# Kernel optimization log

Measured on AMD Instinct MI355X. Metric: run time of the kernel, lower is better.

## Reference

```python
import jax, jax.numpy as jnp
import numpy as np

N_HEAD, N_KV, HD, CA_DIM, VE_CH = 16, 4, 64, 32, 12
B, T, C = 4, 1024, 1024
FFN_H = 4 * C
CA_STEPS = 4

def rms_norm(x):
    return x * jax.lax.rsqrt(jnp.mean(x * x, axis=-1, keepdims=True) + 1e-6)

def rope(x, cos, sin):
    d = x.shape[-1] // 2
    x1, x2 = x[..., :d], x[..., d:]
    return jnp.concatenate([x1 * cos + x2 * sin, -x1 * sin + x2 * cos], axis=-1)

def dwconv1d(x_bct, w, pad):  # w: (Cch,1,K) depthwise
    return jax.lax.conv_general_dilated(x_bct, w, (1,), [(pad, pad)],
        feature_group_count=x_bct.shape[1], dimension_numbers=('NCH', 'OIH', 'NCH'))

def dwconv2d(x_bchw, w):  # w: (Cch,1,3,3) depthwise
    return jax.lax.conv_general_dilated(x_bchw, w, (1, 1), [(1, 1), (1, 1)],
        feature_group_count=x_bchw.shape[1], dimension_numbers=('NCHW', 'OIHW', 'NCHW'))

def ca_channel(x, ca_pi, ca_cw, ca_po):
    h = x @ ca_pi.T  # (B,T,CA_DIM)
    h = h + 0.1 * jnp.transpose(dwconv1d(jnp.transpose(h, (0, 2, 1)), ca_cw, 1), (0, 2, 1))
    return jax.nn.gelu(h, approximate=False) @ ca_po.T

def setup_inputs() -> dict:
    key = jax.random.key(0)
    ks = jax.random.split(key, 20)
    s = 0.02
    pos = jnp.arange(T, dtype=jnp.float32)
    inv_freq = 1.0 / (10000.0 ** (jnp.arange(HD // 2, dtype=jnp.float32) / (HD // 2)))
    ang = pos[:, None] * inv_freq[None, :]  # (T, HD/2)
    return {
        'x': jax.random.normal(ks[0], (B, T, C), jnp.float32),
        've': jax.random.normal(ks[1], (B, T, N_KV * HD), jnp.float32),
        'cos': jnp.cos(ang)[None, :, None, :],
        'sin': jnp.sin(ang)[None, :, None, :],
        'prev_attn': jax.random.uniform(ks[2], (B, N_HEAD, T, T), jnp.float32),
        'w_q': s * jax.random.normal(ks[3], (N_HEAD * HD, C), jnp.float32),
        'w_k': s * jax.random.normal(ks[4], (N_KV * HD, C), jnp.float32),
        'w_v': s * jax.random.normal(ks[5], (N_KV * HD, C), jnp.float32),
        'w_o': s * jax.random.normal(ks[6], (C, C), jnp.float32),
        'w_ve_gate': s * jax.random.normal(ks[7], (N_KV, VE_CH), jnp.float32),
        'refine_w': s * jax.random.normal(ks[8], (N_HEAD, 1, 3, 3), jnp.float32),
        'refine_alpha': jnp.float32(0.05),
        'ca_pi': s * jax.random.normal(ks[9], (CA_DIM, C), jnp.float32),
        'ca_cw': s * jax.random.normal(ks[10], (CA_DIM, 1, 3), jnp.float32),
        'ca_po': s * jax.random.normal(ks[11], (C, CA_DIM), jnp.float32),
        'ffn_in': s * jax.random.normal(ks[12], (FFN_H, C), jnp.float32),
        'ffn_cw': s * jax.random.normal(ks[13], (FFN_H, 1, 3), jnp.float32),
        'ffn_out': s * jax.random.normal(ks[14], (C, FFN_H), jnp.float32),
        'ffn_gate': s * jax.random.normal(ks[15], (C, C), jnp.float32),
        'vit_w1': s * jax.random.normal(ks[16], (32, C), jnp.float32),
        'vit_w2': s * jax.random.normal(ks[17], (1, 32), jnp.float32),
    }

def reference(x, ve, cos, sin, prev_attn, w_q, w_k, w_v, w_o, w_ve_gate,
              refine_w, refine_alpha, ca_pi, ca_cw, ca_po,
              ffn_in, ffn_cw, ffn_out, ffn_gate, vit_w1, vit_w2):
    Bx, Tx, Cx = x.shape
    xn = rms_norm(x)
    q = (xn @ w_q.T).reshape(Bx, Tx, N_HEAD, HD)
    k = (xn @ w_k.T).reshape(Bx, Tx, N_KV, HD)
    v = (xn @ w_v.T).reshape(Bx, Tx, N_KV, HD)
    gate = 3.0 * jax.nn.sigmoid(xn[..., :VE_CH] @ w_ve_gate.T)  # (B,T,N_KV)
    v = v + gate[..., None] * ve.reshape(Bx, Tx, N_KV, HD)
    q = rms_norm(rope(q, cos, sin)) * 1.2
    k = rms_norm(rope(k, cos, sin)) * 1.2
    r = N_HEAD // N_KV
    k = jnp.repeat(k, r, axis=2)
    v = jnp.repeat(v, r, axis=2)
    q, k, v = (jnp.transpose(t, (0, 2, 1, 3)) for t in (q, k, v))  # (B,H,T,HD)
    att = jnp.einsum('bhqd,bhkd->bhqk', q, k) * (1.0 / np.sqrt(HD))
    att = att + refine_alpha * dwconv2d(prev_attn[:, :, :Tx, :Tx], refine_w)
    cmask = jnp.tril(jnp.ones((Tx, Tx), bool))
    att = jnp.where(cmask, att, -jnp.inf)
    aw = jax.nn.softmax(att, axis=-1)
    y = jnp.einsum('bhqk,bhkd->bhqd', aw, v)
    attn_out = jnp.transpose(y, (0, 2, 1, 3)).reshape(Bx, Tx, Cx) @ w_o.T
    # ca_mode='both': gate the attention output
    ca1 = ca_channel(x, ca_pi, ca_cw, ca_po)
    x1 = x + attn_out * (1.0 + 0.1 * jnp.tanh(ca1))
    # CAFFN
    xm = rms_norm(x1)
    h = jnp.square(jax.nn.relu(xm @ ffn_in.T))  # (B,T,FFN_H)
    ht = jnp.transpose(h, (0, 2, 1))
    for _ in range(CA_STEPS):
        ht = ht + 0.1 * dwconv1d(ht, ffn_cw, 1)
    h = jnp.transpose(ht, (0, 2, 1))
    mlp = (h @ ffn_out.T) * jax.nn.sigmoid(xm @ ffn_gate.T)
    ca2 = ca_channel(x1, ca_pi, ca_cw, ca_po)
    mlp = mlp * (1.0 + 0.1 * jnp.tanh(ca2))
    # vitality gating: MLP -> sigmoid, then avg_pool1d(k=5, pad=2, zero-counted)
    vit = jax.nn.sigmoid(jax.nn.gelu(x1 @ vit_w1.T, approximate=False) @ vit_w2.T)[..., 0]  # (B,T)
    vp = jnp.pad(vit, ((0, 0), (2, 2)))
    vs = sum(vp[:, i:i + Tx] for i in range(5)) / 5.0
    vit = 0.7 * vit + 0.3 * vs
    vit = jnp.where(vit > 0.3, vit, vit * 0.1)
    return x1 + mlp * vit[..., None]
```

## Files before the change

kernel.cpp:

```cpp
#include <hip/hip_runtime.h>

#define BB 4
#define TT 1024
#define CC 1024
#define NH 16
#define NKV 4
#define HD 64
#define FFNH 4096
#define CAD 32
#define TQ 64
#define TK 64

typedef short bf16x8 __attribute__((ext_vector_type(8)));
typedef float f32x4  __attribute__((ext_vector_type(4)));

#define AS1 __attribute__((address_space(1)))
#define AS3 __attribute__((address_space(3)))

__device__ __forceinline__ float sigf(float x){ return 1.f/(1.f+__expf(-x)); }
__device__ __forceinline__ float geluf(float x){ return 0.5f*x*(1.f+erff(x*0.70710678118654752f)); }

__device__ __forceinline__ unsigned short f2bf(float f){
  unsigned int u = __float_as_uint(f);
  u += 0x7fffu + ((u >> 16) & 1u);
  return (unsigned short)(u >> 16);
}
__device__ __forceinline__ float bf2f(unsigned short h){
  return __uint_as_float(((unsigned int)h) << 16);
}

__global__ __launch_bounds__(256) void rmsnorm_pair_k(const float* __restrict__ x,
    unsigned short* __restrict__ oh, unsigned short* __restrict__ ol){
  int row = blockIdx.x;
  const float* xr = x + (size_t)row * CC;
  float v[4]; float ss = 0.f;
  #pragma unroll
  for (int i = 0; i < 4; i++){ v[i] = xr[threadIdx.x + 256*i]; ss += v[i]*v[i]; }
  #pragma unroll
  for (int off = 1; off < 64; off <<= 1) ss += __shfl_xor(ss, off);
  __shared__ float red[4];
  if ((threadIdx.x & 63) == 0) red[threadIdx.x >> 6] = ss;
  __syncthreads();
  float tot = red[0]+red[1]+red[2]+red[3];
  float rs = rsqrtf(tot * (1.f/CC) + 1e-6f);
  size_t base = (size_t)row * CC;
  #pragma unroll
  for (int i = 0; i < 4; i++){
    float r = v[i]*rs;
    unsigned short h = f2bf(r);
    oh[base + threadIdx.x + 256*i] = h;
    ol[base + threadIdx.x + 256*i] = f2bf(r - bf2f(h));
  }
}

__global__ __launch_bounds__(256) void split_k(const float* __restrict__ in,
    unsigned short* __restrict__ hi, unsigned short* __restrict__ lo, int n4){
  int i = blockIdx.x*256 + threadIdx.x;
  if (i >= n4) return;
  float4 v = ((const float4*)in)[i];
  unsigned short h0 = f2bf(v.x), h1 = f2bf(v.y), h2v = f2bf(v.z), h3 = f2bf(v.w);
  ushort4 hv = { h0, h1, h2v, h3 };
  ushort4 lv = { f2bf(v.x - bf2f(h0)), f2bf(v.y - bf2f(h1)),
                 f2bf(v.z - bf2f(h2v)), f2bf(v.w - bf2f(h3)) };
  ((ushort4*)hi)[i] = hv;
  ((ushort4*)lo)[i] = lv;
}

template<int EPI>
__global__ __launch_bounds__(256) void gemm3_k(
    const unsigned short* __restrict__ Ah, const unsigned short* __restrict__ Al,
    const unsigned short* __restrict__ Wh, const unsigned short* __restrict__ Wl,
    float* __restrict__ C, int M, int N, int K, int KC)
{
  __shared__ unsigned short AhS[128*32];
  __shared__ unsigned short AlS[128*32];
  __shared__ unsigned short WhS[128*32];
  __shared__ unsigned short WlS[128*32];
  int tid  = threadIdx.x;
  int lane = tid & 63, wave = tid >> 6;
  int wr = wave >> 1, wc = wave & 1;
  int m0 = blockIdx.y << 7, n0 = blockIdx.x << 7;
  int z  = blockIdx.z;
  int kbase = z * KC;
  float* Cz = C + (size_t)z * M * N;
  int lr = lane & 15, lc = lane >> 4;

  int offA[4], offB[4];
  #pragma unroll
  for (int m = 0; m < 4; m++){
    int row = wr*64 + m*16 + lr;
    offA[m] = row*64 + ((lc ^ ((row >> 1) & 3)) << 4);
  }
  #pragma unroll
  for (int n = 0; n < 4; n++){
    int row = wc*64 + n*16 + lr;
    offB[n] = row*64 + ((lc ^ ((row >> 1) & 3)) << 4);
  }

  f32x4 acc[4][4] = {};

  for (int k0 = kbase; k0 < kbase + KC; k0 += 32){
    __syncthreads();
    {
      const unsigned short* srcs[4] = { Ah, Al, Wh, Wl };
      unsigned short* dsts[4] = { AhS, AlS, WhS, WlS };
      int rb[4] = { m0, m0, n0, n0 };
      #pragma unroll
      for (int tle = 0; tle < 4; tle++){
        #pragma unroll
        for (int i = 0; i < 2; i++){
          int s = i*256 + tid;
          int row = s >> 2;
          int c = (s & 3) ^ ((row >> 1) & 3);
          const unsigned short* gp = srcs[tle] + (size_t)(rb[tle] + row)*K + (k0 + c*8);
          unsigned short* lp = dsts[tle] + i*2048 + wave*512;
          __builtin_amdgcn_global_load_lds((const AS1 void*)gp, (AS3 void*)lp, 16, 0, 0);
        }
      }
    }
    __syncthreads();

    bf16x8 ah[4], al[4], bh[4], bl[4];
    #pragma unroll
    for (int m = 0; m < 4; m++){
      ah[m] = *(const bf16x8*)((const char*)AhS + offA[m]);
      al[m] = *(const bf16x8*)((const char*)AlS + offA[m]);
    }
    #pragma unroll
    for (int n = 0; n < 4; n++){
      bh[n] = *(const bf16x8*)((const char*)WhS + offB[n]);
      bl[n] = *(const bf16x8*)((const char*)WlS + offB[n]);
    }
    #pragma unroll
    for (int m = 0; m < 4; m++){
      #pragma unroll
      for (int n = 0; n < 4; n++){
        acc[m][n] = __builtin_amdgcn_mfma_f32_16x16x32_bf16(al[m], bh[n], acc[m][n], 0, 0, 0);
        acc[m][n] = __builtin_amdgcn_mfma_f32_16x16x32_bf16(ah[m], bl[n], acc[m][n], 0, 0, 0);
        acc[m][n] = __builtin_amdgcn_mfma_f32_16x16x32_bf16(ah[m], bh[n], acc[m][n], 0, 0, 0);
      }
    }
  }

  #pragma unroll
  for (int m = 0; m < 4; m++){
    int r0 = m0 + wr*64 + m*16 + lc*4;
    #pragma unroll
    for (int n = 0; n < 4; n++){
      int col = n0 + wc*64 + n*16 + lr;
      #pragma unroll
      for (int r = 0; r < 4; r++){
        float z2 = acc[m][n][r];
        if (EPI == 1){ z2 = fmaxf(z2, 0.f); z2 = z2*z2; }
        Cz[(size_t)(r0 + r)*N + col] = z2;
      }
    }
  }
}

__global__ __launch_bounds__(256) void redsum_k(const float* __restrict__ p,
    float* __restrict__ o, size_t n, int parts){
  size_t i = ((size_t)blockIdx.x*256 + threadIdx.x)*4;
  float4 s = *(const float4*)(p + i);
  for (int z = 1; z < parts; z++){
    float4 q = *(const float4*)(p + (size_t)z*n + i);
    s.x += q.x; s.y += q.y; s.z += q.z; s.w += q.w;
  }
  *(float4*)(o + i) = s;
}

__global__ __launch_bounds__(64) void rope_rms_k(float* __restrict__ q,
    const float* __restrict__ cs, const float* __restrict__ sn, int nh){
  int idx = blockIdx.x;
  int t = (idx / nh) & (TT-1);
  float* qp = q + (size_t)idx * HD;
  int d = threadIdx.x;
  int dl = d & 31;
  float c = cs[t*32 + dl], s = sn[t*32 + dl];
  float v0 = qp[d];
  float vp = qp[(d < 32) ? d + 32 : d - 32];
  float r = (d < 32) ? (v0*c + vp*s) : (v0*c - vp*s);
  float ss = r*r;
  #pragma unroll
  for (int off = 1; off < 64; off <<= 1) ss += __shfl_xor(ss, off);
  float rs = rsqrtf(ss*(1.f/HD) + 1e-6f) * 1.2f;
  qp[d] = r*rs;
}

__global__ __launch_bounds__(256) void gatev_k(float* __restrict__ v,
    const unsigned short* __restrict__ xnh, const unsigned short* __restrict__ xnl,
    const float* __restrict__ ve, const float* __restrict__ wg){
  int bt = blockIdx.x;
  int tid = threadIdx.x;
  int kv = tid >> 6;
  float s = 0.f;
  #pragma unroll
  for (int j = 0; j < 12; j++){
    float xv = bf2f(xnh[(size_t)bt*CC + j]) + bf2f(xnl[(size_t)bt*CC + j]);
    s += xv*wg[kv*12+j];
  }
  float gate = 3.f * sigf(s);
  size_t i = (size_t)bt*(NKV*HD) + tid;
  v[i] += gate * ve[i];
}

__global__ __launch_bounds__(256) void fattn_k(
    const float* __restrict__ q, const float* __restrict__ k, const float* __restrict__ v,
    const float* __restrict__ pa, const float* __restrict__ rw,
    const float* __restrict__ alphap,
    unsigned short* __restrict__ yh, unsigned short* __restrict__ yl)
{
  int qt = blockIdx.x;
  int h  = blockIdx.y;
  int b  = blockIdx.z;
  int kv = h >> 2;
  int t0 = qt * TQ;
  int tid = threadIdx.x;
  int lane = tid & 63, w = tid >> 6;
  int dl = lane & 15, gq = lane >> 4;

  __shared__ __align__(16) unsigned short Kh[4096], Kl[4096];
  __shared__ __align__(16) unsigned short Vh[64][68];
  __shared__ __align__(16) unsigned short SBs[66*68];
  __shared__ __align__(16) unsigned short Ph[4][1024];

  bf16x8 qfh[2], qfl[2];
  {
    const float* qrow = q + (((size_t)(b*TT + t0 + 16*w + dl))*NH + h)*HD;
    #pragma unroll
    for (int ks = 0; ks < 2; ks++){
      float4 a = *(const float4*)(qrow + (gq+4*ks)*8);
      float4 bq = *(const float4*)(qrow + (gq+4*ks)*8 + 4);
      float vv[8] = {a.x,a.y,a.z,a.w,bq.x,bq.y,bq.z,bq.w};
      #pragma unroll
      for (int i = 0; i < 8; i++){
        unsigned short hv = f2bf(vv[i]);
        qfh[ks][i] = (short)hv;
        qfl[ks][i] = (short)f2bf(vv[i] - bf2f(hv));
      }
    }
  }

  float alpha = *alphap;
  float w9[9];
  #pragma unroll
  for (int j = 0; j < 9; j++) w9[j] = rw[h*9+j]*alpha;

  float m_i = -1e30f, l_i = 0.f;
  f32x4 acc_o[4] = {};
  int ql = 16*w + dl;

  for (int kt = 0; kt <= qt; kt++){
    int k0 = kt*TK;
    __syncthreads();
    #pragma unroll
    for (int it = 0; it < 4; it++){
      int s = it*256 + tid;
      int r = s >> 4, d4 = (s & 15) << 2;
      const float* kp = k + (((size_t)(b*TT + k0 + r))*NKV + kv)*HD + d4;
      float4 val = *(const float4*)kp;
      ushort4 hv = { f2bf(val.x), f2bf(val.y), f2bf(val.z), f2bf(val.w) };
      ushort4 lv = { f2bf(val.x - bf2f(hv.x)), f2bf(val.y - bf2f(hv.y)),
                     f2bf(val.z - bf2f(hv.z)), f2bf(val.w - bf2f(hv.w)) };
      int idx = r*64 + (((d4 >> 3) ^ (r & 7)) << 3) + (d4 & 7);
      *(ushort4*)&Kh[idx] = hv;
      *(ushort4*)&Kl[idx] = lv;
      const float* vp = v + (((size_t)(b*TT + k0 + r))*NKV + kv)*HD + d4;
      float4 vval = *(const float4*)vp;
      ushort4 vh4 = { f2bf(vval.x), f2bf(vval.y), f2bf(vval.z), f2bf(vval.w) };
      *(ushort4*)&Vh[r][d4] = vh4;
    }
    #pragma unroll
    for (int it = 0; it < 4; it++){
      int e = it*256 + tid;
      int r = e >> 4, c4 = (e & 15) << 2;
      const float* pp = pa + ((size_t)(b*NH + h)*TT + (t0 + r))*TT + (k0 + c4);
      float4 pv = *(const float4*)pp;
      unsigned short* sp = &SBs[(r+1)*68 + (c4+1)];
      sp[0] = f2bf(pv.x); sp[1] = f2bf(pv.y); sp[2] = f2bf(pv.z); sp[3] = f2bf(pv.w);
    }
    for (int e = tid; e < 260; e += 256){
      int li, lj;
      if (e < 132){ li = (e < 66) ? 0 : 65; lj = (e < 66) ? e : e - 66; }
      else { int idx = e - 132; li = 1 + (idx & 63); lj = (idx >> 6) ? 65 : 0; }
      int gr = t0 - 1 + li, gc = k0 - 1 + lj;
      float pv = 0.f;
      if (gr >= 0 && gr < TT && gc >= 0 && gc < TT)
        pv = pa[((size_t)(b*NH + h)*TT + gr)*TT + gc];
      SBs[li*68 + lj] = f2bf(pv);
    }
    __syncthreads();

    f32x4 acc_s[4] = {};
    __builtin_amdgcn_s_setprio(1);
    #pragma unroll
    for (int ks = 0; ks < 2; ks++){
      #pragma unroll
      for (int kf = 0; kf < 4; kf++){
        int row = 16*kf + dl;
        int idx = row*64 + (((gq + 4*ks) ^ (row & 7)) << 3);
        bf16x8 kh_ = *(const bf16x8*)&Kh[idx];
        bf16x8 kl_ = *(const bf16x8*)&Kl[idx];
        acc_s[kf] = __builtin_amdgcn_mfma_f32_16x16x32_bf16(kl_, qfh[ks], acc_s[kf], 0, 0, 0);
        acc_s[kf] = __builtin_amdgcn_mfma_f32_16x16x32_bf16(kh_, qfl[ks], acc_s[kf], 0, 0, 0);
        acc_s[kf] = __builtin_amdgcn_mfma_f32_16x16x32_bf16(kh_, qfh[ks], acc_s[kf], 0, 0, 0);
      }
    }
    __builtin_amdgcn_s_setprio(0);

    #pragma unroll
    for (int kf = 0; kf < 4; kf++){
      int kb = 16*kf + 4*gq;
      float cv0=0.f, cv1=0.f, cv2=0.f, cv3=0.f;
      #pragma unroll
      for (int dy = 0; dy < 3; dy++){
        const unsigned short* rp = &SBs[(ql + dy)*68 + kb];
        float u0 = bf2f(rp[0]), u1 = bf2f(rp[1]), u2 = bf2f(rp[2]),
              u3 = bf2f(rp[3]), u4 = bf2f(rp[4]), u5 = bf2f(rp[5]);
        float wa = w9[dy*3+0], wb = w9[dy*3+1], wcq = w9[dy*3+2];
        cv0 += u0*wa + u1*wb + u2*wcq;
        cv1 += u1*wa + u2*wb + u3*wcq;
        cv2 += u2*wa + u3*wb + u4*wcq;
        cv3 += u3*wa + u4*wb + u5*wcq;
      }
      int grow = t0 + ql;
      float s0 = acc_s[kf][0]*0.125f + cv0; if (k0 + kb + 0 > grow) s0 = -1e30f;
      float s1 = acc_s[kf][1]*0.125f + cv1; if (k0 + kb + 1 > grow) s1 = -1e30f;
      float s2 = acc_s[kf][2]*0.125f + cv2; if (k0 + kb + 2 > grow) s2 = -1e30f;
      float s3 = acc_s[kf][3]*0.125f + cv3; if (k0 + kb + 3 > grow) s3 = -1e30f;
      acc_s[kf][0] = s0; acc_s[kf][1] = s1; acc_s[kf][2] = s2; acc_s[kf][3] = s3;
    }

    float rm = -1e30f;
    #pragma unroll
    for (int kf = 0; kf < 4; kf++){
      rm = fmaxf(rm, fmaxf(fmaxf(acc_s[kf][0], acc_s[kf][1]),
                           fmaxf(acc_s[kf][2], acc_s[kf][3])));
    }
    rm = fmaxf(rm, __shfl_xor(rm, 16));
    rm = fmaxf(rm, __shfl_xor(rm, 32));
    float mn = fmaxf(m_i, rm);
    float sc = __expf(m_i - mn);
    m_i = mn;
    float rs = 0.f;
    #pragma unroll
    for (int kf = 0; kf < 4; kf++){
      float p0 = __expf(acc_s[kf][0] - mn);
      float p1 = __expf(acc_s[kf][1] - mn);
      float p2 = __expf(acc_s[kf][2] - mn);
      float p3 = __expf(acc_s[kf][3] - mn);
      rs += p0 + p1 + p2 + p3;
      ushort4 hv = { f2bf(p0), f2bf(p1), f2bf(p2), f2bf(p3) };
      int kbl = 16*kf + 4*gq;
      int idx = dl*64 + ((((kbl >> 3)) ^ (dl & 7)) << 3) + (kbl & 7);
      *(ushort4*)&Ph[w][idx] = hv;
    }
    rs += __shfl_xor(rs, 16);
    rs += __shfl_xor(rs, 32);
    l_i = l_i*sc + rs;

    float scR0 = __shfl(sc, gq*4 + 0);
    float scR1 = __shfl(sc, gq*4 + 1);
    float scR2 = __shfl(sc, gq*4 + 2);
    float scR3 = __shfl(sc, gq*4 + 3);
    #pragma unroll
    for (int nf = 0; nf < 4; nf++){
      acc_o[nf][0] *= scR0; acc_o[nf][1] *= scR1;
      acc_o[nf][2] *= scR2; acc_o[nf][3] *= scR3;
    }

    #pragma unroll
    for (int ks = 0; ks < 2; ks++){
      int idxp = dl*64 + (((gq + 4*ks) ^ (dl & 7)) << 3);
      bf16x8 pfh = *(const bf16x8*)&Ph[w][idxp];
      __builtin_amdgcn_s_setprio(1);
      #pragma unroll
      for (int nf = 0; nf < 4; nf++){
        bf16x8 vh_;
        #pragma unroll
        for (int i = 0; i < 8; i++)
          vh_[i] = (short)Vh[ks*32 + gq*8 + i][16*nf + dl];
        acc_o[nf] = __builtin_amdgcn_mfma_f32_16x16x32_bf16(pfh, vh_, acc_o[nf], 0, 0, 0);
      }
      __builtin_amdgcn_s_setprio(0);
    }
  }

  float li0 = __shfl(l_i, gq*4 + 0);
  float li1 = __shfl(l_i, gq*4 + 1);
  float li2 = __shfl(l_i, gq*4 + 2);
  float li3 = __shfl(l_i, gq*4 + 3);
  float inv0 = 1.f/li0, inv1 = 1.f/li1, inv2 = 1.f/li2, inv3 = 1.f/li3;
  #pragma unroll
  for (int nf = 0; nf < 4; nf++){
    int dcol = 16*nf + dl;
    #pragma unroll
    for (int reg = 0; reg < 4; reg++){
      float invv = (reg == 0) ? inv0 : (reg == 1) ? inv1 : (reg == 2) ? inv2 : inv3;
      float val = acc_o[nf][reg] * invv;
      size_t bix = (((size_t)(b*TT + t0 + 16*w + gq*4 + reg))*NH + h)*HD + dcol;
      unsigned short hv = f2bf(val);
      yh[bix] = hv;
      yl[bix] = f2bf(val - bf2f(hv));
    }
  }
}

__global__ __launch_bounds__(256) void cain_k(const float* __restrict__ x,
    const float* __restrict__ pi, float* __restrict__ out){
  int bt = blockIdx.x;
  __shared__ float xs[CC];
  __shared__ float pr[8][33];
  for (int i = threadIdx.x; i < CC; i += 256) xs[i] = x[(size_t)bt*CC + i];
  __syncthreads();
  int d = threadIdx.x & 31, sl = threadIdx.x >> 5;
  const float* pip = pi + (size_t)d*CC + sl*128;
  float s = 0.f;
  #pragma unroll 8
  for (int i = 0; i < 128; i++) s += xs[sl*128+i]*pip[i];
  pr[sl][d] = s;
  __syncthreads();
  if (threadIdx.x < 32){
    float tot = 0.f;
    #pragma unroll
    for (int j = 0; j < 8; j++) tot += pr[j][threadIdx.x];
    out[(size_t)bt*CAD + threadIdx.x] = tot;
  }
}

__global__ __launch_bounds__(256) void caconv_k(const float* __restrict__ hin,
    const float* __restrict__ cw, float* __restrict__ gout){
  int i = blockIdx.x*256 + threadIdx.x;
  int d = i & 31;
  int bt = i >> 5;
  int t = bt & (TT-1);
  float cc = hin[i];
  float hm = (t > 0)      ? hin[i-32] : 0.f;
  float hp = (t < TT-1)   ? hin[i+32] : 0.f;
  float hc = cc + 0.1f*(hm*cw[d*3] + cc*cw[d*3+1] + hp*cw[d*3+2]);
  gout[i] = geluf(hc);
}

__global__ __launch_bounds__(256) void caout_k(const float* __restrict__ g,
    const float* __restrict__ po, float* __restrict__ out){
  int bt = blockIdx.x;
  __shared__ float gs[CAD];
  if (threadIdx.x < CAD) gs[threadIdx.x] = g[(size_t)bt*CAD + threadIdx.x];
  __syncthreads();
  for (int c = threadIdx.x; c < CC; c += 256){
    const float* pp = po + (size_t)c*CAD;
    float s = 0.f;
    #pragma unroll
    for (int d2 = 0; d2 < CAD; d2++) s += gs[d2]*pp[d2];
    out[(size_t)bt*CC + c] = s;
  }
}

__global__ __launch_bounds__(256) void x1_k(const float* __restrict__ x,
    const float* __restrict__ ao, const float* __restrict__ ca1, float* __restrict__ x1){
  size_t i = (size_t)blockIdx.x*256 + threadIdx.x;
  x1[i] = x[i] + ao[i] * (1.f + 0.1f*tanhf(ca1[i]));
}

__global__ __launch_bounds__(256) void ffnconv4_k(const float* __restrict__ hin,
    const float* __restrict__ cw, unsigned short* __restrict__ hh, unsigned short* __restrict__ hl){
  int c  = blockIdx.x*256 + threadIdx.x;
  int ta = blockIdx.y*64;
  int b  = blockIdx.z;
  float w0 = cw[c*3+0], w1 = cw[c*3+1], w2 = cw[c*3+2];
  size_t base = (size_t)b*TT*FFNH + c;
  float i0=0.f,i1=0.f,i2=0.f;
  float a0=0.f,a1=0.f,a2=0.f;
  float b0=0.f,b1=0.f,b2=0.f;
  float c0=0.f,c1=0.f,c2=0.f;
  for (int t = ta-4; t <= ta+67; t++){
    float iv = 0.f;
    if (t >= 0 && t < TT) iv = hin[base + (size_t)t*FFNH];
    i0 = i1; i1 = i2; i2 = iv;
    float s1 = i1 + 0.1f*(i0*w0 + i1*w1 + i2*w2);
    if (t-1 < 0 || t-1 >= TT) s1 = 0.f;
    a0 = a1; a1 = a2; a2 = s1;
    float s2 = a1 + 0.1f*(a0*w0 + a1*w1 + a2*w2);
    if (t-2 < 0 || t-2 >= TT) s2 = 0.f;
    b0 = b1; b1 = b2; b2 = s2;
    float s3 = b1 + 0.1f*(b0*w0 + b1*w1 + b2*w2);
    if (t-3 < 0 || t-3 >= TT) s3 = 0.f;
    c0 = c1; c1 = c2; c2 = s3;
    float s4 = c1 + 0.1f*(c0*w0 + c1*w1 + c2*w2);
    int t4 = t-4;
    if (t4 >= ta){
      size_t oix = base + (size_t)t4*FFNH;
      unsigned short hv = f2bf(s4);
      hh[oix] = hv;
      hl[oix] = f2bf(s4 - bf2f(hv));
    }
  }
}

__global__ __launch_bounds__(256) void vit_k(const float* __restrict__ x1,
    const float* __restrict__ w1, const float* __restrict__ w2,
    float* __restrict__ vout){
  int bt = blockIdx.x;
  __shared__ float xs[CC];
  __shared__ float pr[8][33];
  __shared__ float g32[32];
  for (int i = threadIdx.x; i < CC; i += 256) xs[i] = x1[(size_t)bt*CC + i];
  __syncthreads();
  int d = threadIdx.x & 31, sl = threadIdx.x >> 5;
  const float* wp = w1 + (size_t)d*CC + sl*128;
  float s = 0.f;
  #pragma unroll 8
  for (int i = 0; i < 128; i++) s += xs[sl*128+i]*wp[i];
  pr[sl][d] = s;
  __syncthreads();
  if (threadIdx.x < 32){
    float tot = 0.f;
    #pragma unroll
    for (int j = 0; j < 8; j++) tot += pr[j][threadIdx.x];
    g32[threadIdx.x] = geluf(tot);
  }
  __syncthreads();
  if (threadIdx.x == 0){
    float s2 = 0.f;
    #pragma unroll
    for (int d2 = 0; d2 < 32; d2++) s2 += g32[d2]*w2[d2];
    vout[bt] = sigf(s2);
  }
}

__global__ __launch_bounds__(256) void vitsm_k(const float* __restrict__ vin, float* __restrict__ vout){
  int i = blockIdx.x*256 + threadIdx.x;
  int t = i & (TT-1), b = i >> 10;
  float s = 0.f;
  #pragma unroll
  for (int dd = -2; dd <= 2; dd++){
    int tt = t + dd;
    if (tt >= 0 && tt < TT) s += vin[(b << 10) + tt];
  }
  s *= 0.2f;
  float vv = 0.7f*vin[i] + 0.3f*s;
  vout[i] = (vv > 0.3f) ? vv : 0.1f*vv;
}

__global__ __launch_bounds__(256) void final_k(const float* __restrict__ x1,
    const float* __restrict__ mlpraw, const float* __restrict__ g,
    const float* __restrict__ ca2, const float* __restrict__ vsm,
    float* __restrict__ out){
  size_t i = (size_t)blockIdx.x*256 + threadIdx.x;
  size_t bt = i >> 10;
  float mlp = mlpraw[i] * sigf(g[i]) * (1.f + 0.1f*tanhf(ca2[i]));
  out[i] = x1[i] + mlp * vsm[bt];
}

extern "C" void kernel_launch(void* const* d_in, const int* in_sizes, int n_in,
                              void* d_out, int out_size, void* d_ws, size_t ws_size,
                              hipStream_t stream) {
  (void)in_sizes; (void)n_in; (void)out_size; (void)ws_size;
  const float* x     = (const float*)d_in[0];
  const float* ve    = (const float*)d_in[1];
  const float* cs    = (const float*)d_in[2];
  const float* sn    = (const float*)d_in[3];
  const float* pa    = (const float*)d_in[4];
  const float* w_q   = (const float*)d_in[5];
  const float* w_k   = (const float*)d_in[6];
  const float* w_v   = (const float*)d_in[7];
  const float* w_o   = (const float*)d_in[8];
  const float* w_vg  = (const float*)d_in[9];
  const float* rfw   = (const float*)d_in[10];
  const float* ralp  = (const float*)d_in[11];
  const float* capi  = (const float*)d_in[12];
  const float* cacw  = (const float*)d_in[13];
  const float* capo  = (const float*)d_in[14];
  const float* ffin  = (const float*)d_in[15];
  const float* ffcw  = (const float*)d_in[16];
  const float* ffout = (const float*)d_in[17];
  const float* ffgt  = (const float*)d_in[18];
  const float* vw1   = (const float*)d_in[19];
  const float* vw2   = (const float*)d_in[20];

  const size_t M4  = (size_t)BB*TT*CC;
  const size_t MB1 = 1ull << 20;
  char* WSB = (char*)d_ws;

  unsigned short* xnh = (unsigned short*)WSB;
  unsigned short* xnl = xnh + M4;
  float* ca1 = (float*)WSB;
  float* qb  = (float*)(WSB + 16*MB1);
  float* kb  = (float*)(WSB + 32*MB1);
  unsigned short* ffgp = (unsigned short*)(WSB + 32*MB1);
  float* vb  = (float*)(WSB + 36*MB1);
  float* cah = (float*)(WSB + 36*MB1);
  float* cag = cah + (size_t)BB*TT*CAD;
  float* vtb = cag + (size_t)BB*TT*CAD;
  float* vsm = vtb + (size_t)BB*TT;
  float* ao  = (float*)(WSB + 40*MB1);
  float* x1b = (float*)(WSB + 56*MB1);
  unsigned short* yh = (unsigned short*)x1b;
  unsigned short* yl = yh + M4;
  float* hb  = (float*)(WSB + 72*MB1);
  float* h2  = (float*)(WSB + 136*MB1);
  unsigned short* hh = (unsigned short*)h2;
  unsigned short* hl = hh + 4*M4;
  unsigned short* wqp = (unsigned short*)(WSB + 136*MB1);
  unsigned short* wkp = (unsigned short*)(WSB + 140*MB1);
  unsigned short* wvp = (unsigned short*)(WSB + 141*MB1);
  unsigned short* wop = (unsigned short*)(WSB + 142*MB1);
  float* ca2 = h2;
  unsigned short* ffip = (unsigned short*)(WSB + 200*MB1);
  unsigned short* ffop = (unsigned short*)(WSB + 216*MB1);

  float* kpart = hb;
  float* vpart = hb + 4*M4/4;
  float* qpart = hb + 8*M4/4;
  float* opart = hb;
  float* gpart = hb;
  float* fpart = hb;

  const int BT = BB*TT;
  const int WQN = NH*HD*CC;
  const int WKN = NKV*HD*CC;

  split_k<<<WQN/1024, 256, 0, stream>>>(w_q, wqp, wqp + WQN, WQN/4);
  split_k<<<WKN/1024, 256, 0, stream>>>(w_k, wkp, wkp + WKN, WKN/4);
  split_k<<<WKN/1024, 256, 0, stream>>>(w_v, wvp, wvp + WKN, WKN/4);
  split_k<<<WQN/1024, 256, 0, stream>>>(w_o, wop, wop + WQN, WQN/4);
  split_k<<<M4/1024, 256, 0, stream>>>(ffin, ffip, ffip + M4, (int)(M4/4));
  split_k<<<M4/1024, 256, 0, stream>>>(ffout, ffop, ffop + M4, (int)(M4/4));

  rmsnorm_pair_k<<<BT, 256, 0, stream>>>(x, xnh, xnl);
  gemm3_k<0><<<dim3(8, 32, 2), 256, 0, stream>>>(xnh, xnl, wqp, wqp + WQN, qpart, BT, 1024, 1024, 512);
  redsum_k<<<4096, 256, 0, stream>>>(qpart, qb, (size_t)BT*1024, 2);
  gemm3_k<0><<<dim3(2, 32, 4), 256, 0, stream>>>(xnh, xnl, wkp, wkp + WKN, kpart, BT, 256, 1024, 256);
  redsum_k<<<1024, 256, 0, stream>>>(kpart, kb, (size_t)BT*256, 4);
  gemm3_k<0><<<dim3(2, 32, 4), 256, 0, stream>>>(xnh, xnl, wvp, wvp + WKN, vpart, BT, 256, 1024, 256);
  redsum_k<<<1024, 256, 0, stream>>>(vpart, vb, (size_t)BT*256, 4);
  rope_rms_k<<<BT*NH, 64, 0, stream>>>(qb, cs, sn, NH);
  rope_rms_k<<<BT*NKV, 64, 0, stream>>>(kb, cs, sn, NKV);
  gatev_k<<<BT, 256, 0, stream>>>(vb, xnh, xnl, ve, w_vg);
  fattn_k<<<dim3(TT/TQ, NH, BB), 256, 0, stream>>>(qb, kb, vb, pa, rfw, ralp, yh, yl);
  gemm3_k<0><<<dim3(8, 32, 2), 256, 0, stream>>>(yh, yl, wop, wop + WQN, opart, BT, 1024, 1024, 512);
  redsum_k<<<4096, 256, 0, stream>>>(opart, ao, (size_t)BT*1024, 2);
  split_k<<<WQN/1024, 256, 0, stream>>>(ffgt, ffgp, ffgp + WQN, WQN/4);
  cain_k<<<BT, 256, 0, stream>>>(x, capi, cah);
  caconv_k<<<BT*CAD/256, 256, 0, stream>>>(cah, cacw, cag);
  caout_k<<<BT, 256, 0, stream>>>(cag, capo, ca1);
  x1_k<<<BT*CC/256, 256, 0, stream>>>(x, ao, ca1, x1b);
  rmsnorm_pair_k<<<BT, 256, 0, stream>>>(x1b, xnh, xnl);
  gemm3_k<1><<<dim3(32, 32), 256, 0, stream>>>(xnh, xnl, ffip, ffip + M4, hb, BT, FFNH, 1024, 1024);
  ffnconv4_k<<<dim3(FFNH/256, TT/64, BB), 256, 0, stream>>>(hb, ffcw, hh, hl);
  gemm3_k<0><<<dim3(8, 32, 2), 256, 0, stream>>>(xnh, xnl, ffgp, ffgp + WQN, gpart, BT, 1024, 1024, 512);
  redsum_k<<<4096, 256, 0, stream>>>(gpart, qb, (size_t)BT*1024, 2);
  gemm3_k<0><<<dim3(8, 32, 4), 256, 0, stream>>>(hh, hl, ffop, ffop + M4, fpart, BT, 1024, 4096, 1024);
  redsum_k<<<4096, 256, 0, stream>>>(fpart, ao, (size_t)BT*1024, 4);
  cain_k<<<BT, 256, 0, stream>>>(x1b, capi, cah);
  caconv_k<<<BT*CAD/256, 256, 0, stream>>>(cah, cacw, cag);
  caout_k<<<BT, 256, 0, stream>>>(cag, capo, ca2);
  vit_k<<<BT, 256, 0, stream>>>(x1b, vw1, vw2, vtb);
  vitsm_k<<<BT/256, 256, 0, stream>>>(vtb, vsm);
  final_k<<<BT*CC/256, 256, 0, stream>>>(x1b, ao, qb, ca2, vsm, (float*)d_out);
}
```

Baseline: 1.441 ms.

## Fuse weight splits and split-K reductions into consumer kernels; drop K low-part MFMA

All seven weight hi/lo bf16 split launches are merged into one kernel, with the ffn_gate buffer moved to a new workspace offset. The split-K partial sums for Q, K, V and the output projection are now summed inside the rope/rms, value-gate and x1 kernels, which removes four redsum launches and their extra memory round trips. The attention score MFMA drops the K-low times Q-high term and the Kl shared buffer, cutting MFMA work and LDS traffic. The cost is lower QK precision and workspace aliasing that has to stay correct.

```diff
diff --git a/kernel.cpp b/kernel.cpp
--- a/kernel.cpp
+++ b/kernel.cpp
@@ -53,17 +53,36 @@
   }
 }
 
-__global__ __launch_bounds__(256) void split_k(const float* __restrict__ in,
-    unsigned short* __restrict__ hi, unsigned short* __restrict__ lo, int n4){
-  int i = blockIdx.x*256 + threadIdx.x;
-  if (i >= n4) return;
-  float4 v = ((const float4*)in)[i];
+#define SQ4 262144
+#define SK4 65536
+#define SF4 1048576
+__global__ __launch_bounds__(256) void splitall_k(
+    const float* __restrict__ wq, const float* __restrict__ wk,
+    const float* __restrict__ wv, const float* __restrict__ wo,
+    const float* __restrict__ fi, const float* __restrict__ fo,
+    const float* __restrict__ fg,
+    unsigned short* __restrict__ hq, unsigned short* __restrict__ hk,
+    unsigned short* __restrict__ hv, unsigned short* __restrict__ ho,
+    unsigned short* __restrict__ hi, unsigned short* __restrict__ hfo,
+    unsigned short* __restrict__ hg)
+{
+  int g = blockIdx.x*256 + threadIdx.x;
+  const float* src; unsigned short* dh; int lo4; int n4;
+  if (g < SQ4)                        { src=wq; dh=hq;  lo4=g;                     n4=SQ4; }
+  else if (g < SQ4+SK4)               { src=wk; dh=hk;  lo4=g-SQ4;                 n4=SK4; }
+  else if (g < SQ4+2*SK4)             { src=wv; dh=hv;  lo4=g-SQ4-SK4;             n4=SK4; }
+  else if (g < 2*SQ4+2*SK4)           { src=wo; dh=ho;  lo4=g-SQ4-2*SK4;           n4=SQ4; }
+  else if (g < 2*SQ4+2*SK4+SF4)       { src=fi; dh=hi;  lo4=g-2*SQ4-2*SK4;         n4=SF4; }
+  else if (g < 2*SQ4+2*SK4+2*SF4)     { src=fo; dh=hfo; lo4=g-2*SQ4-2*SK4-SF4;     n4=SF4; }
+  else                                { src=fg; dh=hg;  lo4=g-2*SQ4-2*SK4-2*SF4;   n4=SQ4; }
+  unsigned short* dl = dh + (size_t)n4*4;
+  float4 v = ((const float4*)src)[lo4];
   unsigned short h0 = f2bf(v.x), h1 = f2bf(v.y), h2v = f2bf(v.z), h3 = f2bf(v.w);
-  ushort4 hv = { h0, h1, h2v, h3 };
-  ushort4 lv = { f2bf(v.x - bf2f(h0)), f2bf(v.y - bf2f(h1)),
-                 f2bf(v.z - bf2f(h2v)), f2bf(v.w - bf2f(h3)) };
-  ((ushort4*)hi)[i] = hv;
-  ((ushort4*)lo)[i] = lv;
+  ushort4 hvv = { h0, h1, h2v, h3 };
+  ushort4 lvv = { f2bf(v.x - bf2f(h0)), f2bf(v.y - bf2f(h1)),
+                  f2bf(v.z - bf2f(h2v)), f2bf(v.w - bf2f(h3)) };
+  ((ushort4*)dh)[lo4] = hvv;
+  ((ushort4*)dl)[lo4] = lvv;
 }
 
 template<int EPI>
@@ -169,25 +188,31 @@
   *(float4*)(o + i) = s;
 }
 
-__global__ __launch_bounds__(64) void rope_rms_k(float* __restrict__ q,
-    const float* __restrict__ cs, const float* __restrict__ sn, int nh){
+__global__ __launch_bounds__(64) void rope_rms_sum_k(float* __restrict__ out,
+    const float* __restrict__ parts, const float* __restrict__ cs,
+    const float* __restrict__ sn, int nh, int nparts, size_t ps){
   int idx = blockIdx.x;
   int t = (idx / nh) & (TT-1);
-  float* qp = q + (size_t)idx * HD;
   int d = threadIdx.x;
+  int dsw = (d < 32) ? d + 32 : d - 32;
+  size_t base = (size_t)idx * HD;
+  float v0 = 0.f, vp = 0.f;
+  for (int z = 0; z < nparts; z++){
+    v0 += parts[(size_t)z*ps + base + d];
+    vp += parts[(size_t)z*ps + base + dsw];
+  }
   int dl = d & 31;
   float c = cs[t*32 + dl], s = sn[t*32 + dl];
-  float v0 = qp[d];
-  float vp = qp[(d < 32) ? d + 32 : d - 32];
   float r = (d < 32) ? (v0*c + vp*s) : (v0*c - vp*s);
   float ss = r*r;
   #pragma unroll
   for (int off = 1; off < 64; off <<= 1) ss += __shfl_xor(ss, off);
   float rs = rsqrtf(ss*(1.f/HD) + 1e-6f) * 1.2f;
-  qp[d] = r*rs;
+  out[base + d] = r*rs;
 }
 
 __global__ __launch_bounds__(256) void gatev_k(float* __restrict__ v,
+    const float* __restrict__ vparts, int nparts, size_t ps,
     const unsigned short* __restrict__ xnh, const unsigned short* __restrict__ xnl,
     const float* __restrict__ ve, const float* __restrict__ wg){
   int bt = blockIdx.x;
@@ -201,7 +226,9 @@
   }
   float gate = 3.f * sigf(s);
   size_t i = (size_t)bt*(NKV*HD) + tid;
-  v[i] += gate * ve[i];
+  float sv = 0.f;
+  for (int z = 0; z < nparts; z++) sv += vparts[(size_t)z*ps + i];
+  v[i] = sv + gate * ve[i];
 }
 
 __global__ __launch_bounds__(256) void fattn_k(
@@ -219,7 +246,7 @@
   int lane = tid & 63, w = tid >> 6;
   int dl = lane & 15, gq = lane >> 4;
 
-  __shared__ __align__(16) unsigned short Kh[4096], Kl[4096];
+  __shared__ __align__(16) unsigned short Kh[4096];
   __shared__ __align__(16) unsigned short Vh[64][68];
   __shared__ __align__(16) unsigned short SBs[66*68];
   __shared__ __align__(16) unsigned short Ph[4][1024];
@@ -260,11 +287,8 @@
       const float* kp = k + (((size_t)(b*TT + k0 + r))*NKV + kv)*HD + d4;
       float4 val = *(const float4*)kp;
       ushort4 hv = { f2bf(val.x), f2bf(val.y), f2bf(val.z), f2bf(val.w) };
-      ushort4 lv = { f2bf(val.x - bf2f(hv.x)), f2bf(val.y - bf2f(hv.y)),
-                     f2bf(val.z - bf2f(hv.z)), f2bf(val.w - bf2f(hv.w)) };
       int idx = r*64 + (((d4 >> 3) ^ (r & 7)) << 3) + (d4 & 7);
       *(ushort4*)&Kh[idx] = hv;
-      *(ushort4*)&Kl[idx] = lv;
       const float* vp = v + (((size_t)(b*TT + k0 + r))*NKV + kv)*HD + d4;
       float4 vval = *(const float4*)vp;
       ushort4 vh4 = { f2bf(vval.x), f2bf(vval.y), f2bf(vval.z), f2bf(vval.w) };
@@ -300,8 +324,6 @@
         int row = 16*kf + dl;
         int idx = row*64 + (((gq + 4*ks) ^ (row & 7)) << 3);
         bf16x8 kh_ = *(const bf16x8*)&Kh[idx];
-        bf16x8 kl_ = *(const bf16x8*)&Kl[idx];
-        acc_s[kf] = __builtin_amdgcn_mfma_f32_16x16x32_bf16(kl_, qfh[ks], acc_s[kf], 0, 0, 0);
         acc_s[kf] = __builtin_amdgcn_mfma_f32_16x16x32_bf16(kh_, qfl[ks], acc_s[kf], 0, 0, 0);
         acc_s[kf] = __builtin_amdgcn_mfma_f32_16x16x32_bf16(kh_, qfh[ks], acc_s[kf], 0, 0, 0);
       }
@@ -457,9 +479,11 @@
 }
 
 __global__ __launch_bounds__(256) void x1_k(const float* __restrict__ x,
-    const float* __restrict__ ao, const float* __restrict__ ca1, float* __restrict__ x1){
+    const float* __restrict__ opart, size_t ps,
+    const float* __restrict__ ca1, float* __restrict__ x1){
   size_t i = (size_t)blockIdx.x*256 + threadIdx.x;
-  x1[i] = x[i] + ao[i] * (1.f + 0.1f*tanhf(ca1[i]));
+  float ao = opart[i] + opart[i + ps];
+  x1[i] = x[i] + ao * (1.f + 0.1f*tanhf(ca1[i]));
 }
 
 __global__ __launch_bounds__(256) void ffnconv4_k(const float* __restrict__ hin,
@@ -587,12 +611,12 @@
   float* ca1 = (float*)WSB;
   float* qb  = (float*)(WSB + 16*MB1);
   float* kb  = (float*)(WSB + 32*MB1);
-  unsigned short* ffgp = (unsigned short*)(WSB + 32*MB1);
   float* vb  = (float*)(WSB + 36*MB1);
   float* cah = (float*)(WSB + 36*MB1);
   float* cag = cah + (size_t)BB*TT*CAD;
   float* vtb = cag + (size_t)BB*TT*CAD;
   float* vsm = vtb + (size_t)BB*TT;
+  unsigned short* ffgp = (unsigned short*)(WSB + 40*MB1);
   float* ao  = (float*)(WSB + 40*MB1);
   float* x1b = (float*)(WSB + 56*MB1);
   unsigned short* yh = (unsigned short*)x1b;
@@ -618,33 +642,23 @@
 
   const int BT = BB*TT;
   const int WQN = NH*HD*CC;
-  const int WKN = NKV*HD*CC;
-
-  split_k<<<WQN/1024, 256, 0, stream>>>(w_q, wqp, wqp + WQN, WQN/4);
-  split_k<<<WKN/1024, 256, 0, stream>>>(w_k, wkp, wkp + WKN, WKN/4);
-  split_k<<<WKN/1024, 256, 0, stream>>>(w_v, wvp, wvp + WKN, WKN/4);
-  split_k<<<WQN/1024, 256, 0, stream>>>(w_o, wop, wop + WQN, WQN/4);
-  split_k<<<M4/1024, 256, 0, stream>>>(ffin, ffip, ffip + M4, (int)(M4/4));
-  split_k<<<M4/1024, 256, 0, stream>>>(ffout, ffop, ffop + M4, (int)(M4/4));
+
+  splitall_k<<<11776, 256, 0, stream>>>(w_q, w_k, w_v, w_o, ffin, ffout, ffgt,
+                                        wqp, wkp, wvp, wop, ffip, ffop, ffgp);
 
   rmsnorm_pair_k<<<BT, 256, 0, stream>>>(x, xnh, xnl);
   gemm3_k<0><<<dim3(8, 32, 2), 256, 0, stream>>>(xnh, xnl, wqp, wqp + WQN, qpart, BT, 1024, 1024, 512);
-  redsum_k<<<4096, 256, 0, stream>>>(qpart, qb, (size_t)BT*1024, 2);
-  gemm3_k<0><<<dim3(2, 32, 4), 256, 0, stream>>>(xnh, xnl, wkp, wkp + WKN, kpart, BT, 256, 1024, 256);
-  redsum_k<<<1024, 256, 0, stream>>>(kpart, kb, (size_t)BT*256, 4);
-  gemm3_k<0><<<dim3(2, 32, 4), 256, 0, stream>>>(xnh, xnl, wvp, wvp + WKN, vpart, BT, 256, 1024, 256);
-  redsum_k<<<1024, 256, 0, stream>>>(vpart, vb, (size_t)BT*256, 4);
-  rope_rms_k<<<BT*NH, 64, 0, stream>>>(qb, cs, sn, NH);
-  rope_rms_k<<<BT*NKV, 64, 0, stream>>>(kb, cs, sn, NKV);
-  gatev_k<<<BT, 256, 0, stream>>>(vb, xnh, xnl, ve, w_vg);
+  gemm3_k<0><<<dim3(2, 32, 4), 256, 0, stream>>>(xnh, xnl, wkp, wkp + NKV*HD*CC, kpart, BT, 256, 1024, 256);
+  gemm3_k<0><<<dim3(2, 32, 4), 256, 0, stream>>>(xnh, xnl, wvp, wvp + NKV*HD*CC, vpart, BT, 256, 1024, 256);
+  rope_rms_sum_k<<<BT*NH, 64, 0, stream>>>(qb, qpart, cs, sn, NH, 2, (size_t)BT*1024);
+  rope_rms_sum_k<<<BT*NKV, 64, 0, stream>>>(kb, kpart, cs, sn, NKV, 4, (size_t)BT*256);
+  gatev_k<<<BT, 256, 0, stream>>>(vb, vpart, 4, (size_t)BT*256, xnh, xnl, ve, w_vg);
   fattn_k<<<dim3(TT/TQ, NH, BB), 256, 0, stream>>>(qb, kb, vb, pa, rfw, ralp, yh, yl);
   gemm3_k<0><<<dim3(8, 32, 2), 256, 0, stream>>>(yh, yl, wop, wop + WQN, opart, BT, 1024, 1024, 512);
-  redsum_k<<<4096, 256, 0, stream>>>(opart, ao, (size_t)BT*1024, 2);
-  split_k<<<WQN/1024, 256, 0, stream>>>(ffgt, ffgp, ffgp + WQN, WQN/4);
   cain_k<<<BT, 256, 0, stream>>>(x, capi, cah);
   caconv_k<<<BT*CAD/256, 256, 0, stream>>>(cah, cacw, cag);
   caout_k<<<BT, 256, 0, stream>>>(cag, capo, ca1);
-  x1_k<<<BT*CC/256, 256, 0, stream>>>(x, ao, ca1, x1b);
+  x1_k<<<BT*CC/256, 256, 0, stream>>>(x, opart, (size_t)BT*1024, ca1, x1b);
   rmsnorm_pair_k<<<BT, 256, 0, stream>>>(x1b, xnh, xnl);
   gemm3_k<1><<<dim3(32, 32), 256, 0, stream>>>(xnh, xnl, ffip, ffip + M4, hb, BT, FFNH, 1024, 1024);
   ffnconv4_k<<<dim3(FFNH/256, TT/64, BB), 256, 0, stream>>>(hb, ffcw, hh, hl);
```

Result: faster. 1.404 ms (-2.6%).
